# Optimization experiments

Hardware: AMD Instinct MI355X
Metric: run time of the kernel (lower is better)

The kernel has to match this reference:

```python
import jax, jax.numpy as jnp
import numpy as np

N_HEADS = 16
HIDDEN = 1024
HEAD = HIDDEN // N_HEADS


def setup_inputs() -> dict:
    key = jax.random.key(0)
    ks = jax.random.split(key, 11)
    B, S, H = 2, 2048, HIDDEN
    s = 1.0 / np.sqrt(H)
    return {
        "query": jax.random.normal(ks[0], (B, S, H), jnp.float32),
        "key": jax.random.normal(ks[1], (B, S, H), jnp.float32),
        "value": jax.random.normal(ks[2], (B, S, H), jnp.float32),
        "Wq": jax.random.normal(ks[3], (H, H), jnp.float32) * s,
        "bq": jnp.zeros((H,), jnp.float32),
        "Wk": jax.random.normal(ks[4], (H, H), jnp.float32) * s,
        "bk": jnp.zeros((H,), jnp.float32),
        "Wv": jax.random.normal(ks[5], (H, H), jnp.float32) * s,
        "bv": jnp.zeros((H,), jnp.float32),
        "Wo": jax.random.normal(ks[6], (H, H), jnp.float32) * s,
        "bo": jnp.zeros((H,), jnp.float32),
    }


def reference(query, key, value, Wq, bq, Wk, bk, Wv, bv, Wo, bo):
    B, Sq, H = query.shape
    Sk = key.shape[1]
    # QKV projections, split heads: [B, n_heads, S, head]
    q = (query @ Wq + bq).reshape(B, Sq, N_HEADS, HEAD).transpose(0, 2, 1, 3)
    k = (key @ Wk + bk).reshape(B, Sk, N_HEADS, HEAD).transpose(0, 2, 1, 3)
    v = (value @ Wv + bv).reshape(B, Sk, N_HEADS, HEAD).transpose(0, 2, 1, 3)
    # scaled dot-product attention (no mask, dropout p=0)
    scores = jnp.einsum("bhqd,bhkd->bhqk", q, k) / np.sqrt(HEAD).astype(np.float32)
    attn = jax.nn.softmax(scores, axis=-1)
    out = jnp.einsum("bhqk,bhkd->bhqd", attn, v)
    out = out.transpose(0, 2, 1, 3).reshape(B, Sq, H)
    return out @ Wo + bo
```

## Files before the change

### kernel.cpp

```cpp
#include <hip/hip_runtime.h>
#include <hip/hip_bf16.h>
#include <stdint.h>

typedef unsigned short u16;
typedef short bf16x8 __attribute__((ext_vector_type(8)));
typedef float f32x4 __attribute__((ext_vector_type(4)));

#define DEVI static __device__ __forceinline__

#if __has_builtin(__builtin_amdgcn_exp2f)
#define EXP2F(x) __builtin_amdgcn_exp2f(x)
#else
#define EXP2F(x) exp2f(x)
#endif

DEVI u16 f2bf(float f) {
  union { float f; uint32_t u; } v; v.f = f;
  uint32_t u = v.u;
  u += 0x7fffu + ((u >> 16) & 1u);
  return (u16)(u >> 16);
}
DEVI uint32_t pk2bf(float lo, float hi) {
  __hip_bfloat162 h = __float22bfloat162_rn(float2{lo, hi});
  union { __hip_bfloat162 h; uint32_t u; } v; v.h = h; return v.u;
}

DEVI void async16(const void* g, const void* l) {
  __builtin_amdgcn_global_load_lds(
      (const __attribute__((address_space(1))) void*)g,
      (__attribute__((address_space(3))) void*)l, 16, 0, 0);
}

DEVI f32x4 mfma16(bf16x8 a, bf16x8 b, f32x4 c) {
  return __builtin_amdgcn_mfma_f32_16x16x32_bf16(a, b, c, 0, 0, 0);
}

#define CSC 0.18033688011112042f

__global__ void prep(const float* __restrict__ q, const float* __restrict__ k,
                     const float* __restrict__ v,
                     const float* __restrict__ Wq, const float* __restrict__ Wk,
                     const float* __restrict__ Wv, const float* __restrict__ Wo,
                     u16* __restrict__ XB, u16* __restrict__ WT) {
  __shared__ u16 tile[64 * 68];
  const int bid = blockIdx.x, t = threadIdx.x;
  if (bid < 12288) {
    const int z = bid >> 12, x = bid & 4095;
    const float* src = (z == 0) ? q : (z == 1) ? k : v;
    const int i = (x * 256 + t) * 4;
    float4 f = *(const float4*)(src + i);
    ushort4 o;
    o.x = f2bf(f.x); o.y = f2bf(f.y); o.z = f2bf(f.z); o.w = f2bf(f.w);
    *(ushort4*)(XB + (size_t)z * 4194304 + i) = o;
  } else {
    const int j = bid - 12288;
    const int z = j >> 8, rem = j & 255;
    const float* W = (z == 0) ? Wq : (z == 1) ? Wk : (z == 2) ? Wv : Wo;
    u16* out = WT + (size_t)z * 1048576;
    const int R0 = (rem >> 4) * 64, C0 = (rem & 15) * 64;
#pragma unroll
    for (int it = 0; it < 16; ++it) {
      int jj = it * 256 + t;
      int r = jj >> 6, c = jj & 63;
      tile[r * 68 + c] = f2bf(W[(size_t)(R0 + r) * 1024 + C0 + c]);
    }
    __syncthreads();
#pragma unroll
    for (int it = 0; it < 16; ++it) {
      int jj = it * 256 + t;
      int c = jj >> 6, r = jj & 63;
      out[(size_t)(C0 + c) * 1024 + R0 + r] = tile[r * 68 + c];
    }
  }
}

DEVI void qstage(const u16* __restrict__ A, const u16* __restrict__ Bt,
                 u16* lA, u16* lB, int m0, int n0, int k0, int t) {
#pragma unroll
  for (int it = 0; it < 4; ++it) {
    int i = it * 256 + t;
    int r = i >> 3, cc = i & 7, c = cc ^ (r & 7);
    async16(A + (size_t)(m0 + r) * 1024 + k0 + c * 8, &lA[i * 8]);
    async16(Bt + (size_t)(n0 + r) * 1024 + k0 + c * 8, &lB[i * 8]);
  }
}

__global__ __launch_bounds__(256, 2)
void qkv_gemm(const u16* __restrict__ XB, const u16* __restrict__ WT,
              const float* __restrict__ bq, const float* __restrict__ bk,
              const float* __restrict__ bv,
              u16* __restrict__ QN, u16* __restrict__ KN, u16* __restrict__ VT) {
  __shared__ u16 smem[32768];
  const int z = blockIdx.y;
  const u16* A  = XB + (size_t)z * 4194304;
  const u16* Bt = WT + (size_t)z * 1048576;
  const float* bias = (z == 0) ? bq : (z == 1) ? bk : bv;
  const int T = blockIdx.x;
  const int m0 = (T & 31) * 128, n0 = (T >> 5) * 128;
  const int t = threadIdx.x, lane = t & 63, w = t >> 6;
  const int quad = lane >> 4, l16 = lane & 15;
  const int wm = (w & 1) * 64, wn = (w >> 1) * 64;

  qstage(A, Bt, smem, smem + 8192, m0, n0, 0, t);

  f32x4 acc[4][4] = {};
  for (int kt = 0; kt < 16; ++kt) {
    asm volatile("s_waitcnt vmcnt(0)" ::: "memory");
    __builtin_amdgcn_s_barrier();
    __builtin_amdgcn_sched_barrier(0);
    if (kt + 1 < 16) {
      u16* nb = smem + ((kt + 1) & 1) * 16384;
      qstage(A, Bt, nb, nb + 8192, m0, n0, (kt + 1) * 64, t);
    }
    const u16* lA = smem + (kt & 1) * 16384;
    const u16* lB = lA + 8192;
#pragma unroll
    for (int ks = 0; ks < 2; ++ks) {
      bf16x8 af[4], bfr[4];
#pragma unroll
      for (int rt = 0; rt < 4; ++rt) {
        int row = wm + rt * 16 + l16;
        af[rt] = *(const bf16x8*)&lA[row * 64 + ((ks * 4 + quad) ^ (row & 7)) * 8];
      }
#pragma unroll
      for (int ct = 0; ct < 4; ++ct) {
        int row = wn + ct * 16 + l16;
        bfr[ct] = *(const bf16x8*)&lB[row * 64 + ((ks * 4 + quad) ^ (row & 7)) * 8];
      }
      __builtin_amdgcn_s_setprio(1);
#pragma unroll
      for (int rt = 0; rt < 4; ++rt)
#pragma unroll
        for (int ct = 0; ct < 4; ++ct)
          acc[rt][ct] = mfma16(bfr[ct], af[rt], acc[rt][ct]);
      __builtin_amdgcn_s_setprio(0);
    }
  }
  __syncthreads();

  if (z < 2) {
    const float scl = (z == 0) ? CSC : 1.0f;
#pragma unroll
    for (int rt = 0; rt < 4; ++rt) {
      int sl = wm + rt * 16 + l16;
#pragma unroll
      for (int ct = 0; ct < 4; ++ct) {
        int nb = wn + ct * 16 + quad * 4;
        float4 b4 = *(const float4*)&bias[n0 + nb];
        ushort4 pk;
        pk.x = f2bf((acc[rt][ct][0] + b4.x) * scl);
        pk.y = f2bf((acc[rt][ct][1] + b4.y) * scl);
        pk.z = f2bf((acc[rt][ct][2] + b4.z) * scl);
        pk.w = f2bf((acc[rt][ct][3] + b4.w) * scl);
        *(ushort4*)&smem[sl * 132 + nb] = pk;
      }
    }
    __syncthreads();
    u16* out = (z == 0) ? QN : KN;
#pragma unroll
    for (int p = 0; p < 8; ++p) {
      int idx = p * 256 + t;
      int row = idx >> 4, chunk = idx & 15;
      *(bf16x8*)&out[(size_t)(m0 + row) * 1024 + n0 + chunk * 8] =
          *(const bf16x8*)&smem[row * 132 + chunk * 8];
    }
  } else {
#pragma unroll
    for (int rt = 0; rt < 4; ++rt) {
      int sl = wm + rt * 16 + l16;
#pragma unroll
      for (int ct = 0; ct < 4; ++ct) {
        int nb = wn + ct * 16 + quad * 4;
        float4 b4 = *(const float4*)&bias[n0 + nb];
        smem[(nb + 0) * 132 + sl] = f2bf(acc[rt][ct][0] + b4.x);
        smem[(nb + 1) * 132 + sl] = f2bf(acc[rt][ct][1] + b4.y);
        smem[(nb + 2) * 132 + sl] = f2bf(acc[rt][ct][2] + b4.z);
        smem[(nb + 3) * 132 + sl] = f2bf(acc[rt][ct][3] + b4.w);
      }
    }
    __syncthreads();
    const int bb = m0 >> 11, sb = m0 & 2047;
#pragma unroll
    for (int p = 0; p < 8; ++p) {
      int idx = p * 256 + t;
      int dl = idx >> 4, chunk = idx & 15;
      int ncol = n0 + dl, hh = ncol >> 6, dd = ncol & 63;
      *(bf16x8*)&VT[((size_t)((bb * 16 + hh) * 64 + dd)) * 2048 + sb + chunk * 8] =
          *(const bf16x8*)&smem[dl * 132 + chunk * 8];
    }
  }
}

__global__ __launch_bounds__(512, 4)
void attn11(const u16* __restrict__ QN, const u16* __restrict__ KN,
            const u16* __restrict__ VT, u16* __restrict__ AO) {
  __shared__ u16 lK[4][64 * 64];
  __shared__ u16 lV[4][64 * 64];
  const int qt0 = blockIdx.x, h = blockIdx.y, b = blockIdx.z;
  const int t = threadIdx.x, lane = t & 63, w = t >> 6;
  const int quad = lane >> 4, l16 = lane & 15;
  const u16* Qg = QN + ((size_t)(b * 2048 + qt0 * 128)) * 1024 + h * 64;
  const u16* Kg = KN + ((size_t)b * 2048) * 1024 + h * 64;
  const u16* Vg = VT + ((size_t)((b * 16 + h) * 64)) * 2048;

  const int sr_r = t >> 3;
  const int sg_r = (sr_r & 0x23) | ((sr_r & 8) << 1) | ((sr_r & 4) << 1) |
                   ((sr_r & 16) >> 2);
  const int sc_c = (t & 7) ^ (sr_r & 7);

  bf16x8 qf[2];
#pragma unroll
  for (int ks = 0; ks < 2; ++ks)
    qf[ks] = *(const bf16x8*)(Qg + (size_t)(w * 16 + l16) * 1024 + ks * 32 + quad * 8);

  const bf16x8 ones = {0x3F80, 0x3F80, 0x3F80, 0x3F80,
                       0x3F80, 0x3F80, 0x3F80, 0x3F80};

  async16(Kg + (size_t)sg_r * 1024 + sc_c * 8, &lK[0][t * 8]);
  async16(Vg + (size_t)sr_r * 2048 + sc_c * 8, &lV[0][t * 8]);
  async16(Kg + (size_t)(64 + sg_r) * 1024 + sc_c * 8, &lK[1][t * 8]);
  async16(Vg + (size_t)sr_r * 2048 + 64 + sc_c * 8, &lV[1][t * 8]);

  f32x4 o[4] = {};
  f32x4 ls = {};

  for (int it = 0; it < 16; ++it) {
    const int ta = it * 2;
    asm volatile("s_waitcnt vmcnt(0)" ::: "memory");
    __builtin_amdgcn_s_barrier();
    __builtin_amdgcn_sched_barrier(0);

    if (it + 1 < 16) {
      const int kb0 = (ta + 2) * 64, nb0 = (ta + 2) & 3;
      async16(Kg + (size_t)(kb0 + sg_r) * 1024 + sc_c * 8, &lK[nb0][t * 8]);
      async16(Vg + (size_t)sr_r * 2048 + kb0 + sc_c * 8, &lV[nb0][t * 8]);
      const int kb1 = (ta + 3) * 64, nb1 = (ta + 3) & 3;
      async16(Kg + (size_t)(kb1 + sg_r) * 1024 + sc_c * 8, &lK[nb1][t * 8]);
      async16(Vg + (size_t)sr_r * 2048 + kb1 + sc_c * 8, &lV[nb1][t * 8]);
    }

    f32x4 sc2[2][4];
    __builtin_amdgcn_s_setprio(1);
#pragma unroll
    for (int u = 0; u < 2; ++u) {
      const u16* Kc = &lK[(ta + u) & 3][0];
#pragma unroll
      for (int st = 0; st < 4; ++st) {
        int row = st * 16 + l16;
        bf16x8 kf0 = *(const bf16x8*)&Kc[row * 64 + ((quad) ^ (row & 7)) * 8];
        bf16x8 kf1 = *(const bf16x8*)&Kc[row * 64 + ((4 + quad) ^ (row & 7)) * 8];
        f32x4 z = {};
        sc2[u][st] = mfma16(kf0, qf[0], z);
        sc2[u][st] = mfma16(kf1, qf[1], sc2[u][st]);
      }
    }
    __builtin_amdgcn_s_setprio(0);

#pragma unroll
    for (int u = 0; u < 2; ++u) {
      union { uint32_t uw[4]; bf16x8 v; } p0, p1;
#pragma unroll
      for (int st = 0; st < 2; ++st) {
        p0.uw[st * 2 + 0] = pk2bf(EXP2F(sc2[u][st][0]), EXP2F(sc2[u][st][1]));
        p0.uw[st * 2 + 1] = pk2bf(EXP2F(sc2[u][st][2]), EXP2F(sc2[u][st][3]));
        p1.uw[st * 2 + 0] = pk2bf(EXP2F(sc2[u][2 + st][0]), EXP2F(sc2[u][2 + st][1]));
        p1.uw[st * 2 + 1] = pk2bf(EXP2F(sc2[u][2 + st][2]), EXP2F(sc2[u][2 + st][3]));
      }
      __builtin_amdgcn_s_setprio(1);
      ls = mfma16(ones, p0.v, ls);
      ls = mfma16(ones, p1.v, ls);
      const u16* Vc = &lV[(ta + u) & 3][0];
#pragma unroll
      for (int dt = 0; dt < 4; ++dt) {
        int row = dt * 16 + l16;
        bf16x8 vf0 = *(const bf16x8*)&Vc[row * 64 + ((quad) ^ (row & 7)) * 8];
        bf16x8 vf1 = *(const bf16x8*)&Vc[row * 64 + ((4 + quad) ^ (row & 7)) * 8];
        o[dt] = mfma16(vf0, p0.v, o[dt]);
        o[dt] = mfma16(vf1, p1.v, o[dt]);
      }
      __builtin_amdgcn_s_setprio(0);
    }
  }

  float inv = 1.0f / ls[0];
  int qglob = qt0 * 128 + w * 16 + l16;
  size_t base = ((size_t)(b * 2048 + qglob)) * 1024 + h * 64;
#pragma unroll
  for (int dt = 0; dt < 4; ++dt) {
    ushort4 pk;
    pk.x = f2bf(o[dt][0] * inv);
    pk.y = f2bf(o[dt][1] * inv);
    pk.z = f2bf(o[dt][2] * inv);
    pk.w = f2bf(o[dt][3] * inv);
    *(ushort4*)&AO[base + dt * 16 + quad * 4] = pk;
  }
}

__global__ __launch_bounds__(256, 3)
void oproj_gemm(const u16* __restrict__ AO, const u16* __restrict__ Bt,
                const float* __restrict__ bias, float* __restrict__ out) {
  __shared__ u16 smem[24576];
  const int T = blockIdx.x;
  const int m0 = (T & 31) * 128, n0 = (T >> 5) * 64;
  const int t = threadIdx.x, lane = t & 63, w = t >> 6;
  const int quad = lane >> 4, l16 = lane & 15;
  const int wm = (w & 1) * 64, wn = (w >> 1) * 32;

  {
    u16* lA = smem; u16* lB = smem + 8192;
#pragma unroll
    for (int it = 0; it < 4; ++it) {
      int i = it * 256 + t;
      int r = i >> 3, cc = i & 7, c = cc ^ (r & 7);
      async16(AO + (size_t)(m0 + r) * 1024 + c * 8, &lA[i * 8]);
    }
#pragma unroll
    for (int it = 0; it < 2; ++it) {
      int i = it * 256 + t;
      int r = i >> 3, cc = i & 7, c = cc ^ (r & 7);
      async16(Bt + (size_t)(n0 + r) * 1024 + c * 8, &lB[i * 8]);
    }
  }

  f32x4 acc[4][2] = {};
  for (int kt = 0; kt < 16; ++kt) {
    asm volatile("s_waitcnt vmcnt(0)" ::: "memory");
    __builtin_amdgcn_s_barrier();
    __builtin_amdgcn_sched_barrier(0);
    if (kt + 1 < 16) {
      const int k0 = (kt + 1) * 64;
      u16* lA = smem + ((kt + 1) & 1) * 12288;
      u16* lB = lA + 8192;
#pragma unroll
      for (int it = 0; it < 4; ++it) {
        int i = it * 256 + t;
        int r = i >> 3, cc = i & 7, c = cc ^ (r & 7);
        async16(AO + (size_t)(m0 + r) * 1024 + k0 + c * 8, &lA[i * 8]);
      }
#pragma unroll
      for (int it = 0; it < 2; ++it) {
        int i = it * 256 + t;
        int r = i >> 3, cc = i & 7, c = cc ^ (r & 7);
        async16(Bt + (size_t)(n0 + r) * 1024 + k0 + c * 8, &lB[i * 8]);
      }
    }
    const u16* lA = smem + (kt & 1) * 12288;
    const u16* lB = lA + 8192;
#pragma unroll
    for (int ks = 0; ks < 2; ++ks) {
      bf16x8 af[4], bfr[2];
#pragma unroll
      for (int rt = 0; rt < 4; ++rt) {
        int row = wm + rt * 16 + l16;
        af[rt] = *(const bf16x8*)&lA[row * 64 + ((ks * 4 + quad) ^ (row & 7)) * 8];
      }
#pragma unroll
      for (int ct = 0; ct < 2; ++ct) {
        int row = wn + ct * 16 + l16;
        bfr[ct] = *(const bf16x8*)&lB[row * 64 + ((ks * 4 + quad) ^ (row & 7)) * 8];
      }
      __builtin_amdgcn_s_setprio(1);
#pragma unroll
      for (int rt = 0; rt < 4; ++rt)
#pragma unroll
        for (int ct = 0; ct < 2; ++ct)
          acc[rt][ct] = mfma16(af[rt], bfr[ct], acc[rt][ct]);
      __builtin_amdgcn_s_setprio(0);
    }
  }

#pragma unroll
  for (int ct = 0; ct < 2; ++ct) {
    int ncol = n0 + wn + ct * 16 + l16;
    float bvv = bias[ncol];
#pragma unroll
    for (int rt = 0; rt < 4; ++rt)
#pragma unroll
      for (int r = 0; r < 4; ++r) {
        int m = m0 + wm + rt * 16 + quad * 4 + r;
        out[(size_t)m * 1024 + ncol] = acc[rt][ct][r] + bvv;
      }
  }
}

extern "C" void kernel_launch(void* const* d_in, const int* in_sizes, int n_in,
                              void* d_out, int out_size, void* d_ws, size_t ws_size,
                              hipStream_t stream) {
  const float* query = (const float*)d_in[0];
  const float* key   = (const float*)d_in[1];
  const float* value = (const float*)d_in[2];
  const float* Wq = (const float*)d_in[3];
  const float* bq = (const float*)d_in[4];
  const float* Wk = (const float*)d_in[5];
  const float* bk = (const float*)d_in[6];
  const float* Wv = (const float*)d_in[7];
  const float* bv = (const float*)d_in[8];
  const float* Wo = (const float*)d_in[9];
  const float* bo = (const float*)d_in[10];
  float* out = (float*)d_out;

  u16* WT = (u16*)d_ws;
  u16* QN = WT + 4 * 1048576;
  u16* KN = QN + 4194304;
  u16* VT = KN + 4194304;
  u16* XB = VT + 4194304;
  u16* AO = XB;

  prep<<<dim3(13312), 256, 0, stream>>>(query, key, value, Wq, Wk, Wv, Wo, XB, WT);
  qkv_gemm<<<dim3(256, 3), 256, 0, stream>>>(XB, WT, bq, bk, bv, QN, KN, VT);
  attn11<<<dim3(16, 16, 2), 512, 0, stream>>>(QN, KN, VT, AO);
  oproj_gemm<<<dim3(512), 256, 0, stream>>>(AO, WT + 3 * 1048576, bo, out);
}
```

Before: 203.0 us.

## Fuse fp32-to-bf16 activation conversion into QKV GEMM A-tile loading

The prep kernel no longer converts query/key/value to bf16 in a separate pass. The QKV GEMM now loads fp32 A tiles into registers, converts them to bf16 and writes them to LDS, while B tiles still use async global-to-LDS loads. This removes one full write and re-read of the bf16 activation copies. In exchange it doubles A-side global read bytes per tile, raises register pressure, and adds an extra barrier per k-step.

```diff
diff --git a/kernel.cpp b/kernel.cpp
--- a/kernel.cpp
+++ b/kernel.cpp
@@ -37,62 +37,39 @@
 
 #define CSC 0.18033688011112042f
 
-__global__ void prep(const float* __restrict__ q, const float* __restrict__ k,
-                     const float* __restrict__ v,
-                     const float* __restrict__ Wq, const float* __restrict__ Wk,
+__global__ void prep(const float* __restrict__ Wq, const float* __restrict__ Wk,
                      const float* __restrict__ Wv, const float* __restrict__ Wo,
-                     u16* __restrict__ XB, u16* __restrict__ WT) {
+                     u16* __restrict__ WT) {
   __shared__ u16 tile[64 * 68];
-  const int bid = blockIdx.x, t = threadIdx.x;
-  if (bid < 12288) {
-    const int z = bid >> 12, x = bid & 4095;
-    const float* src = (z == 0) ? q : (z == 1) ? k : v;
-    const int i = (x * 256 + t) * 4;
-    float4 f = *(const float4*)(src + i);
-    ushort4 o;
-    o.x = f2bf(f.x); o.y = f2bf(f.y); o.z = f2bf(f.z); o.w = f2bf(f.w);
-    *(ushort4*)(XB + (size_t)z * 4194304 + i) = o;
-  } else {
-    const int j = bid - 12288;
-    const int z = j >> 8, rem = j & 255;
-    const float* W = (z == 0) ? Wq : (z == 1) ? Wk : (z == 2) ? Wv : Wo;
-    u16* out = WT + (size_t)z * 1048576;
-    const int R0 = (rem >> 4) * 64, C0 = (rem & 15) * 64;
-#pragma unroll
-    for (int it = 0; it < 16; ++it) {
-      int jj = it * 256 + t;
-      int r = jj >> 6, c = jj & 63;
-      tile[r * 68 + c] = f2bf(W[(size_t)(R0 + r) * 1024 + C0 + c]);
-    }
-    __syncthreads();
-#pragma unroll
-    for (int it = 0; it < 16; ++it) {
-      int jj = it * 256 + t;
-      int c = jj >> 6, r = jj & 63;
-      out[(size_t)(C0 + c) * 1024 + R0 + r] = tile[r * 68 + c];
-    }
-  }
-}
-
-DEVI void qstage(const u16* __restrict__ A, const u16* __restrict__ Bt,
-                 u16* lA, u16* lB, int m0, int n0, int k0, int t) {
-#pragma unroll
-  for (int it = 0; it < 4; ++it) {
-    int i = it * 256 + t;
-    int r = i >> 3, cc = i & 7, c = cc ^ (r & 7);
-    async16(A + (size_t)(m0 + r) * 1024 + k0 + c * 8, &lA[i * 8]);
-    async16(Bt + (size_t)(n0 + r) * 1024 + k0 + c * 8, &lB[i * 8]);
+  const int j = blockIdx.x, t = threadIdx.x;
+  const int z = j >> 8, rem = j & 255;
+  const float* W = (z == 0) ? Wq : (z == 1) ? Wk : (z == 2) ? Wv : Wo;
+  u16* out = WT + (size_t)z * 1048576;
+  const int R0 = (rem >> 4) * 64, C0 = (rem & 15) * 64;
+#pragma unroll
+  for (int it = 0; it < 16; ++it) {
+    int jj = it * 256 + t;
+    int r = jj >> 6, c = jj & 63;
+    tile[r * 68 + c] = f2bf(W[(size_t)(R0 + r) * 1024 + C0 + c]);
+  }
+  __syncthreads();
+#pragma unroll
+  for (int it = 0; it < 16; ++it) {
+    int jj = it * 256 + t;
+    int c = jj >> 6, r = jj & 63;
+    out[(size_t)(C0 + c) * 1024 + R0 + r] = tile[r * 68 + c];
   }
 }
 
 __global__ __launch_bounds__(256, 2)
-void qkv_gemm(const u16* __restrict__ XB, const u16* __restrict__ WT,
+void qkv_gemm(const float* __restrict__ Xq, const float* __restrict__ Xk,
+              const float* __restrict__ Xv, const u16* __restrict__ WT,
               const float* __restrict__ bq, const float* __restrict__ bk,
               const float* __restrict__ bv,
               u16* __restrict__ QN, u16* __restrict__ KN, u16* __restrict__ VT) {
   __shared__ u16 smem[32768];
   const int z = blockIdx.y;
-  const u16* A  = XB + (size_t)z * 4194304;
+  const float* A = (z == 0) ? Xq : (z == 1) ? Xk : Xv;
   const u16* Bt = WT + (size_t)z * 1048576;
   const float* bias = (z == 0) ? bq : (z == 1) ? bk : bv;
   const int T = blockIdx.x;
@@ -101,17 +78,61 @@
   const int quad = lane >> 4, l16 = lane & 15;
   const int wm = (w & 1) * 64, wn = (w >> 1) * 64;
 
-  qstage(A, Bt, smem, smem + 8192, m0, n0, 0, t);
+  float4 Ar[4][2];
+
+#define ALOAD(k0)                                                             \
+  do {                                                                        \
+    _Pragma("unroll")                                                         \
+    for (int it2 = 0; it2 < 4; ++it2) {                                       \
+      int i = it2 * 256 + t;                                                  \
+      int r = i >> 3, cc = i & 7, c = cc ^ (r & 7);                           \
+      const float* src = A + (size_t)(m0 + r) * 1024 + (k0) + c * 8;          \
+      Ar[it2][0] = *(const float4*)src;                                       \
+      Ar[it2][1] = *(const float4*)(src + 4);                                 \
+    }                                                                         \
+  } while (0)
+
+#define BSTAGE(k0, buf)                                                       \
+  do {                                                                        \
+    u16* lB_ = smem + (buf) * 16384 + 8192;                                   \
+    _Pragma("unroll")                                                         \
+    for (int it2 = 0; it2 < 4; ++it2) {                                       \
+      int i = it2 * 256 + t;                                                  \
+      int r = i >> 3, cc = i & 7, c = cc ^ (r & 7);                           \
+      async16(Bt + (size_t)(n0 + r) * 1024 + (k0) + c * 8, &lB_[i * 8]);      \
+    }                                                                         \
+  } while (0)
+
+  ALOAD(0);
+  BSTAGE(0, 0);
 
   f32x4 acc[4][4] = {};
   for (int kt = 0; kt < 16; ++kt) {
     asm volatile("s_waitcnt vmcnt(0)" ::: "memory");
     __builtin_amdgcn_s_barrier();
     __builtin_amdgcn_sched_barrier(0);
+
+    {
+      u16* lAw = smem + (kt & 1) * 16384;
+#pragma unroll
+      for (int it2 = 0; it2 < 4; ++it2) {
+        int i = it2 * 256 + t;
+        uint4 pk;
+        pk.x = pk2bf(Ar[it2][0].x, Ar[it2][0].y);
+        pk.y = pk2bf(Ar[it2][0].z, Ar[it2][0].w);
+        pk.z = pk2bf(Ar[it2][1].x, Ar[it2][1].y);
+        pk.w = pk2bf(Ar[it2][1].z, Ar[it2][1].w);
+        *(uint4*)&lAw[i * 8] = pk;
+      }
+    }
     if (kt + 1 < 16) {
-      u16* nb = smem + ((kt + 1) & 1) * 16384;
-      qstage(A, Bt, nb, nb + 8192, m0, n0, (kt + 1) * 64, t);
-    }
+      ALOAD((kt + 1) * 64);
+      BSTAGE((kt + 1) * 64, (kt + 1) & 1);
+    }
+    asm volatile("s_waitcnt lgkmcnt(0)" ::: "memory");
+    __builtin_amdgcn_s_barrier();
+    __builtin_amdgcn_sched_barrier(0);
+
     const u16* lA = smem + (kt & 1) * 16384;
     const u16* lB = lA + 8192;
 #pragma unroll
@@ -136,6 +157,8 @@
       __builtin_amdgcn_s_setprio(0);
     }
   }
+#undef ALOAD
+#undef BSTAGE
   __syncthreads();
 
   if (z < 2) {
@@ -403,11 +426,11 @@
   u16* QN = WT + 4 * 1048576;
   u16* KN = QN + 4194304;
   u16* VT = KN + 4194304;
-  u16* XB = VT + 4194304;
-  u16* AO = XB;
-
-  prep<<<dim3(13312), 256, 0, stream>>>(query, key, value, Wq, Wk, Wv, Wo, XB, WT);
-  qkv_gemm<<<dim3(256, 3), 256, 0, stream>>>(XB, WT, bq, bk, bv, QN, KN, VT);
+  u16* AO = VT + 4194304;
+
+  prep<<<dim3(1024), 256, 0, stream>>>(Wq, Wk, Wv, Wo, WT);
+  qkv_gemm<<<dim3(256, 3), 256, 0, stream>>>(query, key, value, WT, bq, bk, bv,
+                                             QN, KN, VT);
   attn11<<<dim3(16, 16, 2), 512, 0, stream>>>(QN, KN, VT, AO);
   oproj_gemm<<<dim3(512), 256, 0, stream>>>(AO, WT + 3 * 1048576, bo, out);
 }
```

Measured after the change: 214.2 us. 5.5% more time.
